# Optimization experiments

Measured on AMD Instinct MI355X. Metric: run time of the kernel, lower is better.

Reference implementation:

```python
import jax, jax.numpy as jnp
import numpy as np

B, T, D = 4, 2048, 1024
H, DK = 8, 64
EPS = 1e-6

def _xavier(key, shape):
    fan_in, fan_out = shape[1], shape[0]
    lim = float(np.sqrt(6.0 / (fan_in + fan_out)))
    return jax.random.uniform(key, shape, jnp.float32, -lim, lim)

def setup_inputs() -> dict:
    key = jax.random.key(0)
    ks = jax.random.split(key, 7)
    x = jax.random.normal(ks[0], (B, T, D), jnp.float32)
    W_Q = _xavier(ks[1], (H * DK, D))
    W_K = _xavier(ks[2], (H * DK, D))
    W_V = _xavier(ks[3], (H * DK, D))
    W_g_w = _xavier(ks[4], (H * DK, D))
    W_g_b = jax.random.normal(ks[5], (H * DK,), jnp.float32) * 0.02
    W_O = _xavier(ks[6], (D, H * DK))
    decay_log = jnp.zeros((H,), jnp.float32)
    return {"x": x, "W_Q": W_Q, "W_K": W_K, "W_V": W_V,
            "W_g_w": W_g_w, "W_g_b": W_g_b, "W_O": W_O,
            "decay_log": decay_log}

def _phi(u):
    # ELU + 1 feature map (positive)
    return jax.nn.elu(u) + 1.0

def reference(x, W_Q, W_K, W_V, W_g_w, W_g_b, W_O, decay_log):
    b, t, d = x.shape
    q = _phi((x @ W_Q.T).reshape(b, t, H, DK))
    k = _phi((x @ W_K.T).reshape(b, t, H, DK))
    v = (x @ W_V.T).reshape(b, t, H, DK)
    gamma = jax.nn.sigmoid(decay_log)           # [H]
    g4 = gamma[None, :, None, None]             # [1,H,1,1]
    g3 = gamma[None, :, None]                   # [1,H,1]

    # time-major for scan: [T,B,H,DK]
    qT = jnp.moveaxis(q, 1, 0)
    kT = jnp.moveaxis(k, 1, 0)
    vT = jnp.moveaxis(v, 1, 0)

    S0 = jnp.zeros((b, H, DK, DK), x.dtype)
    z0 = jnp.zeros((b, H, DK), x.dtype)

    def step(carry, inp):
        S, z = carry
        qt, kt, vt = inp
        S = g4 * S + jnp.einsum('bhi,bhj->bhij', kt, vt)
        z = g3 * z + kt
        num = jnp.einsum('bhij,bhi->bhj', S, qt)
        den = jnp.sum(z * qt, axis=-1, keepdims=True) + EPS
        return (S, z), num / den

    _, ys = jax.lax.scan(step, (S0, z0), (qT, kT, vT))  # ys: [T,B,H,DK]
    outputs = jnp.moveaxis(ys, 0, 1)                    # [B,T,H,DK]

    gate = jax.nn.sigmoid(x @ W_g_w.T + W_g_b).reshape(b, t, H, DK)
    y = (outputs * gate).reshape(b, t, H * DK)
    return y @ W_O.T
```

## Files before the change

### kernel.cpp

```cpp
#include <hip/hip_runtime.h>
#include <cstdint>
#include <cstddef>

#define B_   4
#define T_   2048
#define D_   1024
#define H_   8
#define DK_  64
#define HD_  512
#define CH_  64
#define NC_  32
#define EPS_ 1e-6f

typedef __attribute__((ext_vector_type(4))) float f32x4;
typedef __attribute__((ext_vector_type(8))) short s16x8;

__device__ __forceinline__ unsigned short f2bf(float f) {
    unsigned int x = __float_as_uint(f);
    unsigned int r = (x + 0x7FFFu + ((x >> 16) & 1u)) >> 16;
    return (unsigned short)r;
}
__device__ __forceinline__ float bf2f(unsigned short u) {
    return __uint_as_float(((unsigned int)u) << 16);
}
__device__ __forceinline__ void ld4(const float* p, float* o) {
    float4 v = *(const float4*)p; o[0]=v.x; o[1]=v.y; o[2]=v.z; o[3]=v.w;
}
__device__ __forceinline__ void gl_lds16(const unsigned short* g, unsigned short* l) {
    __builtin_amdgcn_global_load_lds(
        (const __attribute__((address_space(1))) unsigned int*)g,
        (__attribute__((address_space(3))) unsigned int*)l, 16, 0, 0);
}

__global__ __launch_bounds__(256) void k_cvt_all(
    const float* __restrict__ x,
    const float* __restrict__ wq, const float* __restrict__ wk,
    const float* __restrict__ wv, const float* __restrict__ wgw,
    const float* __restrict__ wo,
    unsigned short* __restrict__ xb,
    unsigned short* __restrict__ wqb, unsigned short* __restrict__ wkb,
    unsigned short* __restrict__ wvb, unsigned short* __restrict__ wgb,
    unsigned short* __restrict__ wob)
{
    int bid = blockIdx.x;
    const float* src; unsigned short* dst; int idx;
    if (bid < 8192) {
        src = x; dst = xb; idx = bid * 256 + threadIdx.x;
    } else {
        int r = bid - 8192;
        int w = r >> 9;
        idx = (r & 511) * 256 + threadIdx.x;
        switch (w) {
            case 0:  src = wq;  dst = wqb; break;
            case 1:  src = wk;  dst = wkb; break;
            case 2:  src = wv;  dst = wvb; break;
            case 3:  src = wgw; dst = wgb; break;
            default: src = wo;  dst = wob; break;
        }
    }
    float4 v = ((const float4*)src)[idx];
    ushort4 o;
    o.x = f2bf(v.x); o.y = f2bf(v.y); o.z = f2bf(v.z); o.w = f2bf(v.w);
    ((ushort4*)dst)[idx] = o;
}


__global__ __launch_bounds__(512, 2) void k_gemm_qkvg(
    const unsigned short* __restrict__ xb,
    const unsigned short* __restrict__ wqb, const unsigned short* __restrict__ wkb,
    const unsigned short* __restrict__ wvb, const unsigned short* __restrict__ wgb,
    const float* __restrict__ bias,
    unsigned short* __restrict__ qo, unsigned short* __restrict__ ko,
    unsigned short* __restrict__ vo, unsigned short* __restrict__ go)
{
    __shared__ unsigned short As[2][256 * 64];
    __shared__ unsigned short Bs[2][256 * 64];
    const int tid = threadIdx.x;
    const int id  = blockIdx.x;
    const int xcd = id & 7, per = id >> 3;
    const int mtile = xcd * 4 + (per & 3);
    const int ntile = per >> 2;
    const int which = ntile >> 1;
    const int nb    = ntile & 1;
    const int m0    = mtile * 256;
    const int n0    = nb * 256;
    const unsigned short* Wp = (which == 0) ? wqb : (which == 1) ? wkb : (which == 2) ? wvb : wgb;
    unsigned short* Op       = (which == 0) ? qo  : (which == 1) ? ko  : (which == 2) ? vo  : go;
    const int K = D_;
    const int NIT = K / 64;

    const int lane = tid & 63, wave = tid >> 6;
    const int wm = (wave >> 2) * 128, wn = (wave & 3) * 64;
    const int r16 = lane & 15, quad = lane >> 4;
    const int lrow = lane >> 3, lseg = lane & 7;
    const int sseg = lseg ^ lrow;
    const int rx   = r16 & 7;

    f32x4 acc[8][4];
    #pragma unroll
    for (int a = 0; a < 8; a++)
        #pragma unroll
        for (int b = 0; b < 4; b++) acc[a][b] = 0.0f;

    auto stageA = [&](int buf, int ko_) {
        #pragma unroll
        for (int i = 0; i < 4; i++) {
            int chunk = wave * 4 + i;
            int row = chunk * 8 + lrow;
            gl_lds16(xb + (size_t)(m0 + row) * K + ko_ + sseg * 8, &As[buf][chunk * 512]);
        }
    };
    auto stageB = [&](int buf, int ko_) {
        #pragma unroll
        for (int i = 0; i < 4; i++) {
            int chunk = wave * 4 + i;
            int row = chunk * 8 + lrow;
            gl_lds16(Wp + (size_t)(n0 + row) * K + ko_ + sseg * 8, &Bs[buf][chunk * 512]);
        }
    };
    auto rdA = [&](int buf, int row, int gb) -> s16x8 {
        return *(const s16x8*)&As[buf][row * 64 + (((gb + quad) ^ rx) << 3)];
    };
    auto rdB = [&](int buf, int row, int gb) -> s16x8 {
        return *(const s16x8*)&Bs[buf][row * 64 + (((gb + quad) ^ rx) << 3)];
    };

    stageA(0, 0); stageB(0, 0);
    for (int it = 0; it < NIT; ++it) {
        const int buf = it & 1;
        asm volatile("s_waitcnt vmcnt(0)" ::: "memory");
        __builtin_amdgcn_s_barrier();

        s16x8 af[4], bfr[4];
        #pragma unroll
        for (int mt = 0; mt < 4; mt++) af[mt]  = rdA(buf, wm + mt * 16 + r16, 0);
        #pragma unroll
        for (int nt = 0; nt < 4; nt++) bfr[nt] = rdB(buf, wn + nt * 16 + r16, 0);
        if (it + 1 < NIT) stageA(buf ^ 1, (it + 1) * 64);
        __builtin_amdgcn_s_barrier();
        asm volatile("s_waitcnt lgkmcnt(0)" ::: "memory");
        __builtin_amdgcn_sched_barrier(0);
        __builtin_amdgcn_s_setprio(1);
        #pragma unroll
        for (int mt = 0; mt < 4; mt++)
            #pragma unroll
            for (int nt = 0; nt < 4; nt++)
                acc[mt][nt] = __builtin_amdgcn_mfma_f32_16x16x32_bf16(af[mt], bfr[nt], acc[mt][nt], 0, 0, 0);
        __builtin_amdgcn_s_setprio(0);
        __builtin_amdgcn_s_barrier();

        #pragma unroll
        for (int mt = 0; mt < 4; mt++) af[mt] = rdA(buf, wm + (mt + 4) * 16 + r16, 0);
        if (it + 1 < NIT) stageB(buf ^ 1, (it + 1) * 64);
        __builtin_amdgcn_s_barrier();
        asm volatile("s_waitcnt lgkmcnt(0)" ::: "memory");
        __builtin_amdgcn_sched_barrier(0);
        __builtin_amdgcn_s_setprio(1);
        #pragma unroll
        for (int mt = 0; mt < 4; mt++)
            #pragma unroll
            for (int nt = 0; nt < 4; nt++)
                acc[mt + 4][nt] = __builtin_amdgcn_mfma_f32_16x16x32_bf16(af[mt], bfr[nt], acc[mt + 4][nt], 0, 0, 0);
        __builtin_amdgcn_s_setprio(0);
        __builtin_amdgcn_s_barrier();

        #pragma unroll
        for (int mt = 0; mt < 4; mt++) af[mt]  = rdA(buf, wm + mt * 16 + r16, 4);
        #pragma unroll
        for (int nt = 0; nt < 4; nt++) bfr[nt] = rdB(buf, wn + nt * 16 + r16, 4);
        __builtin_amdgcn_s_barrier();
        asm volatile("s_waitcnt lgkmcnt(0)" ::: "memory");
        __builtin_amdgcn_sched_barrier(0);
        __builtin_amdgcn_s_setprio(1);
        #pragma unroll
        for (int mt = 0; mt < 4; mt++)
            #pragma unroll
            for (int nt = 0; nt < 4; nt++)
                acc[mt][nt] = __builtin_amdgcn_mfma_f32_16x16x32_bf16(af[mt], bfr[nt], acc[mt][nt], 0, 0, 0);
        __builtin_amdgcn_s_setprio(0);
        __builtin_amdgcn_s_barrier();

        #pragma unroll
        for (int mt = 0; mt < 4; mt++) af[mt] = rdA(buf, wm + (mt + 4) * 16 + r16, 4);
        __builtin_amdgcn_s_barrier();
        asm volatile("s_waitcnt lgkmcnt(0)" ::: "memory");
        __builtin_amdgcn_sched_barrier(0);
        __builtin_amdgcn_s_setprio(1);
        #pragma unroll
        for (int mt = 0; mt < 4; mt++)
            #pragma unroll
            for (int nt = 0; nt < 4; nt++)
                acc[mt + 4][nt] = __builtin_amdgcn_mfma_f32_16x16x32_bf16(af[mt], bfr[nt], acc[mt + 4][nt], 0, 0, 0);
        __builtin_amdgcn_s_setprio(0);
        __builtin_amdgcn_s_barrier();
    }
    #pragma unroll
    for (int mt = 0; mt < 8; mt++) {
        #pragma unroll
        for (int nt = 0; nt < 4; nt++) {
            int col = n0 + wn + nt * 16 + r16;
            float bv = (which == 3) ? bias[col] : 0.0f;
            #pragma unroll
            for (int r = 0; r < 4; r++) {
                int row = m0 + wm + mt * 16 + quad * 4 + r;
                float v = acc[mt][nt][r];
                if (which <= 1)      v = (v > 0.0f) ? v + 1.0f : __builtin_expf(v);
                else if (which == 3) v = 1.0f / (1.0f + __builtin_expf(-(v + bv)));
                Op[(size_t)row * HD_ + col] = f2bf(v);
            }
        }
    }
}

__global__ __launch_bounds__(512, 2) void k_gemm_out(
    const unsigned short* __restrict__ ogb, const unsigned short* __restrict__ wob,
    float* __restrict__ y)
{
    __shared__ unsigned short As[2][256 * 64];
    __shared__ unsigned short Bs[2][128 * 64];
    const int tid = threadIdx.x;
    const int id  = blockIdx.x;
    const int xcd = id & 7, per = id >> 3;
    const int m0 = (xcd * 4 + (per & 3)) * 256;
    const int n0 = (per >> 2) * 128;
    const int K = HD_;
    const int NIT = K / 64;

    const int lane = tid & 63, wave = tid >> 6;
    const int wm = (wave >> 1) * 64, wn = (wave & 1) * 64;
    const int r16 = lane & 15, quad = lane >> 4;
    const int lrow = lane >> 3, lseg = lane & 7;
    const int sseg = lseg ^ lrow;
    const int rx   = r16 & 7;

    f32x4 acc[4][4];
    #pragma unroll
    for (int a = 0; a < 4; a++)
        #pragma unroll
        for (int b = 0; b < 4; b++) acc[a][b] = 0.0f;

    auto stageA = [&](int buf, int ko_) {
        #pragma unroll
        for (int i = 0; i < 4; i++) {
            int chunk = wave * 4 + i;
            int row = chunk * 8 + lrow;
            gl_lds16(ogb + (size_t)(m0 + row) * K + ko_ + sseg * 8, &As[buf][chunk * 512]);
        }
    };
    auto stageB = [&](int buf, int ko_) {
        #pragma unroll
        for (int i = 0; i < 2; i++) {
            int chunk = wave * 2 + i;
            int row = chunk * 8 + lrow;
            gl_lds16(wob + (size_t)(n0 + row) * K + ko_ + sseg * 8, &Bs[buf][chunk * 512]);
        }
    };
    auto rdA = [&](int buf, int row, int gb) -> s16x8 {
        return *(const s16x8*)&As[buf][row * 64 + (((gb + quad) ^ rx) << 3)];
    };
    auto rdB = [&](int buf, int row, int gb) -> s16x8 {
        return *(const s16x8*)&Bs[buf][row * 64 + (((gb + quad) ^ rx) << 3)];
    };

    stageA(0, 0); stageB(0, 0);
    for (int it = 0; it < NIT; ++it) {
        const int buf = it & 1;
        asm volatile("s_waitcnt vmcnt(0)" ::: "memory");
        __builtin_amdgcn_s_barrier();

        s16x8 af[4], bfr[4];
        #pragma unroll
        for (int mt = 0; mt < 4; mt++) af[mt]  = rdA(buf, wm + mt * 16 + r16, 0);
        #pragma unroll
        for (int nt = 0; nt < 4; nt++) bfr[nt] = rdB(buf, wn + nt * 16 + r16, 0);
        if (it + 1 < NIT) stageA(buf ^ 1, (it + 1) * 64);
        __builtin_amdgcn_s_barrier();
        asm volatile("s_waitcnt lgkmcnt(0)" ::: "memory");
        __builtin_amdgcn_sched_barrier(0);
        __builtin_amdgcn_s_setprio(1);
        #pragma unroll
        for (int mt = 0; mt < 4; mt++)
            #pragma unroll
            for (int nt = 0; nt < 4; nt++)
                acc[mt][nt] = __builtin_amdgcn_mfma_f32_16x16x32_bf16(af[mt], bfr[nt], acc[mt][nt], 0, 0, 0);
        __builtin_amdgcn_s_setprio(0);
        __builtin_amdgcn_s_barrier();

        #pragma unroll
        for (int mt = 0; mt < 4; mt++) af[mt]  = rdA(buf, wm + mt * 16 + r16, 4);
        #pragma unroll
        for (int nt = 0; nt < 4; nt++) bfr[nt] = rdB(buf, wn + nt * 16 + r16, 4);
        if (it + 1 < NIT) stageB(buf ^ 1, (it + 1) * 64);
        __builtin_amdgcn_s_barrier();
        asm volatile("s_waitcnt lgkmcnt(0)" ::: "memory");
        __builtin_amdgcn_sched_barrier(0);
        __builtin_amdgcn_s_setprio(1);
        #pragma unroll
        for (int mt = 0; mt < 4; mt++)
            #pragma unroll
            for (int nt = 0; nt < 4; nt++)
                acc[mt][nt] = __builtin_amdgcn_mfma_f32_16x16x32_bf16(af[mt], bfr[nt], acc[mt][nt], 0, 0, 0);
        __builtin_amdgcn_s_setprio(0);
        __builtin_amdgcn_s_barrier();
    }
    #pragma unroll
    for (int mt = 0; mt < 4; mt++)
        #pragma unroll
        for (int nt = 0; nt < 4; nt++) {
            int col = n0 + wn + nt * 16 + r16;
            #pragma unroll
            for (int r = 0; r < 4; r++) {
                int row = m0 + wm + mt * 16 + quad * 4 + r;
                y[(size_t)row * D_ + col] = acc[mt][nt][r];
            }
        }
}

__global__ __launch_bounds__(256) void k_chunk_sums(
    const unsigned short* __restrict__ Kb, const unsigned short* __restrict__ Vb,
    float* __restrict__ Ssum, float* __restrict__ zsum, const float* __restrict__ decay_log)
{
    __shared__ float kl[CH_ * 68];
    __shared__ float vl[CH_ * 68];
    const int tid = threadIdx.x;
    const int bc  = blockIdx.x;
    const int c   = bc & (NC_ - 1);
    const int bh  = bc >> 5;
    const int h   = bh & (H_ - 1);
    const int b   = bh >> 3;
    const float g  = 1.0f / (1.0f + __builtin_expf(-decay_log[h]));
    const float lg = __builtin_log2f(g);
    const int t0 = c * CH_;

    #pragma unroll
    for (int e = 0; e < 2; e++) {
        int lid = e * 256 + tid;
        int l = lid >> 3, d0 = (lid & 7) * 8;
        float w = __builtin_exp2f((float)(CH_ - 1 - l) * lg);
        size_t gidx = (size_t)(b * T_ + t0 + l) * HD_ + h * DK_ + d0;
        uint4 kraw = *(const uint4*)(Kb + gidx);
        uint4 vraw = *(const uint4*)(Vb + gidx);
        const unsigned short* kp = (const unsigned short*)&kraw;
        const unsigned short* vp = (const unsigned short*)&vraw;
        #pragma unroll
        for (int j = 0; j < 8; j++) {
            kl[l * 68 + d0 + j] = bf2f(kp[j]) * w;
            vl[l * 68 + d0 + j] = bf2f(vp[j]);
        }
    }
    __syncthreads();

    const int ti = tid >> 4, tj = tid & 15;
    const int i0 = ti * 4, j0 = tj * 4;
    float acc[4][4];
    #pragma unroll
    for (int r = 0; r < 4; r++)
        #pragma unroll
        for (int cc = 0; cc < 4; cc++) acc[r][cc] = 0.0f;

    for (int l = 0; l < CH_; l++) {
        float kv[4], vv[4];
        ld4(&kl[l * 68 + i0], kv);
        ld4(&vl[l * 68 + j0], vv);
        #pragma unroll
        for (int r = 0; r < 4; r++)
            #pragma unroll
            for (int cc = 0; cc < 4; cc++) acc[r][cc] += kv[r] * vv[cc];
    }
    size_t base = (size_t)bc * (DK_ * DK_);
    #pragma unroll
    for (int r = 0; r < 4; r++) {
        float4 st = make_float4(acc[r][0], acc[r][1], acc[r][2], acc[r][3]);
        *(float4*)&Ssum[base + (size_t)(i0 + r) * DK_ + j0] = st;
    }
    if (tid < DK_) {
        float s = 0.0f;
        for (int l = 0; l < CH_; l++) s += kl[l * 68 + tid];
        zsum[(size_t)bc * DK_ + tid] = s;
    }
}

__global__ __launch_bounds__(128) void k_chunk_scan(
    float* __restrict__ Ssum, float* __restrict__ zsum, const float* __restrict__ decay_log)
{
    const int tid = threadIdx.x;
    const int grp = blockIdx.x & 31;
    const int bh  = blockIdx.x >> 5;
    const int h   = bh & (H_ - 1);
    const float g  = 1.0f / (1.0f + __builtin_expf(-decay_log[h]));
    const float gC = __builtin_exp2f((float)CH_ * __builtin_log2f(g));
    int elem = grp * 128 + tid;
    float s = 0.0f;
    for (int c = 0; c < NC_; c++) {
        size_t idx = ((size_t)(bh * NC_ + c)) * 4096 + elem;
        float v = Ssum[idx];
        Ssum[idx] = s;
        s = gC * s + v;
    }
    if (grp == 0 && tid < DK_) {
        float z = 0.0f;
        for (int c = 0; c < NC_; c++) {
            size_t idx = ((size_t)(bh * NC_ + c)) * DK_ + tid;
            float v = zsum[idx];
            zsum[idx] = z;
            z = gC * z + v;
        }
    }
}

__global__ __launch_bounds__(256) void k_chunk_out(
    const unsigned short* __restrict__ Qb, const unsigned short* __restrict__ Kb,
    const unsigned short* __restrict__ Vb, const unsigned short* __restrict__ Gb,
    const float* __restrict__ Ssum, const float* __restrict__ zsum,
    unsigned short* __restrict__ OGb, const float* __restrict__ decay_log)
{
    __shared__ float BufA[CH_ * 68];
    __shared__ float BufB[CH_ * 68];
    __shared__ float BufC[CH_ * 68];
    __shared__ float den_l[CH_];
    __shared__ float zp_l[DK_];
    __shared__ float gpow[CH_ + 1];

    const int tid = threadIdx.x;
    const int bc  = blockIdx.x;
    const int c   = bc & (NC_ - 1);
    const int bh  = bc >> 5;
    const int h   = bh & (H_ - 1);
    const int b   = bh >> 3;
    const float g  = 1.0f / (1.0f + __builtin_expf(-decay_log[h]));
    const float lg = __builtin_log2f(g);
    const int t0 = c * CH_;

    if (tid <= CH_) gpow[tid] = __builtin_exp2f((float)tid * lg);
    if (tid < DK_)  zp_l[tid] = zsum[(size_t)bc * DK_ + tid];

    #pragma unroll
    for (int e = 0; e < 2; e++) {
        int lid = e * 256 + tid;
        int l = lid >> 3, d0 = (lid & 7) * 8;
        size_t gidx = (size_t)(b * T_ + t0 + l) * HD_ + h * DK_ + d0;
        uint4 qraw = *(const uint4*)(Qb + gidx);
        uint4 kraw = *(const uint4*)(Kb + gidx);
        const unsigned short* qp = (const unsigned short*)&qraw;
        const unsigned short* kp = (const unsigned short*)&kraw;
        #pragma unroll
        for (int j = 0; j < 8; j++) {
            BufA[(d0 + j) * 68 + l] = bf2f(qp[j]);
            BufB[(d0 + j) * 68 + l] = bf2f(kp[j]);
        }
    }
    {
        size_t base = (size_t)bc * 4096;
        #pragma unroll
        for (int e = 0; e < 4; e++) {
            int flat = (e * 256 + tid) * 4;
            int row = flat >> 6, c0 = flat & 63;
            *(float4*)&BufC[row * 68 + c0] = *(const float4*)&Ssum[base + flat];
        }
    }
    __syncthreads();

    const int ti = tid >> 4, tj = tid & 15;
    const int i0 = ti * 4, j0 = tj * 4;
    float sc[4][4], it[4][4];
    #pragma unroll
    for (int r = 0; r < 4; r++)
        #pragma unroll
        for (int cc = 0; cc < 4; cc++) { sc[r][cc] = 0.0f; it[r][cc] = 0.0f; }

    for (int d = 0; d < DK_; d++) {
        float qv[4], kv[4], sv[4];
        ld4(&BufA[d * 68 + i0], qv);
        ld4(&BufB[d * 68 + j0], kv);
        ld4(&BufC[d * 68 + j0], sv);
        #pragma unroll
        for (int r = 0; r < 4; r++)
            #pragma unroll
            for (int cc = 0; cc < 4; cc++) {
                sc[r][cc] += qv[r] * kv[cc];
                it[r][cc] += qv[r] * sv[cc];
            }
    }
    #pragma unroll
    for (int r = 0; r < 4; r++) {
        int i = i0 + r;
        #pragma unroll
        for (int cc = 0; cc < 4; cc++) {
            int jl = j0 + cc;
            sc[r][cc] = (jl <= i) ? sc[r][cc] * gpow[i - jl] : 0.0f;
            it[r][cc] *= gpow[i + 1];
        }
        float rs = sc[r][0] + sc[r][1] + sc[r][2] + sc[r][3];
        rs += __shfl_xor(rs, 1);
        rs += __shfl_xor(rs, 2);
        rs += __shfl_xor(rs, 4);
        rs += __shfl_xor(rs, 8);
        if (tj == 0) den_l[i] = rs;
    }
    __syncthreads();
    if (tid < DK_) {
        float dp = 0.0f;
        for (int d = 0; d < DK_; d++) dp += BufA[d * 68 + tid] * zp_l[d];
        den_l[tid] += gpow[tid + 1] * dp + EPS_;
    }
    __syncthreads();
    #pragma unroll
    for (int cc = 0; cc < 4; cc++) {
        float4 st = make_float4(sc[0][cc], sc[1][cc], sc[2][cc], sc[3][cc]);
        *(float4*)&BufA[(j0 + cc) * 68 + i0] = st;
    }
    #pragma unroll
    for (int e = 0; e < 2; e++) {
        int lid = e * 256 + tid;
        int l = lid >> 3, d0 = (lid & 7) * 8;
        size_t gidx = (size_t)(b * T_ + t0 + l) * HD_ + h * DK_ + d0;
        uint4 vraw = *(const uint4*)(Vb + gidx);
        const unsigned short* vp = (const unsigned short*)&vraw;
        #pragma unroll
        for (int j = 0; j < 8; j++) BufB[l * 68 + d0 + j] = bf2f(vp[j]);
    }
    __syncthreads();

    float og[4][4];
    #pragma unroll
    for (int r = 0; r < 4; r++)
        #pragma unroll
        for (int cc = 0; cc < 4; cc++) og[r][cc] = it[r][cc];

    for (int jl = 0; jl < CH_; jl++) {
        float scv[4], vv[4];
        ld4(&BufA[jl * 68 + i0], scv);
        ld4(&BufB[jl * 68 + j0], vv);
        #pragma unroll
        for (int r = 0; r < 4; r++)
            #pragma unroll
            for (int cc = 0; cc < 4; cc++) og[r][cc] += scv[r] * vv[cc];
    }
    #pragma unroll
    for (int r = 0; r < 4; r++) {
        int i = i0 + r;
        float rcp = 1.0f / den_l[i];
        size_t gidx = (size_t)(b * T_ + t0 + i) * HD_ + h * DK_ + j0;
        ushort4 graw = *(const ushort4*)(Gb + gidx);
        ushort4 o;
        o.x = f2bf(og[r][0] * rcp * bf2f(graw.x));
        o.y = f2bf(og[r][1] * rcp * bf2f(graw.y));
        o.z = f2bf(og[r][2] * rcp * bf2f(graw.z));
        o.w = f2bf(og[r][3] * rcp * bf2f(graw.w));
        *(ushort4*)(OGb + gidx) = o;
    }
}

extern "C" void kernel_launch(void* const* d_in, const int* in_sizes, int n_in,
                              void* d_out, int out_size, void* d_ws, size_t ws_size,
                              hipStream_t stream)
{
    (void)in_sizes; (void)n_in; (void)out_size; (void)ws_size;
    const float* x         = (const float*)d_in[0];
    const float* W_Q       = (const float*)d_in[1];
    const float* W_K       = (const float*)d_in[2];
    const float* W_V       = (const float*)d_in[3];
    const float* W_gw      = (const float*)d_in[4];
    const float* W_gb      = (const float*)d_in[5];
    const float* W_O       = (const float*)d_in[6];
    const float* decay_log = (const float*)d_in[7];
    float* y = (float*)d_out;

    char* ws = (char*)d_ws;
    size_t off = 0;
    auto alloc = [&](size_t bytes) { void* p = ws + off; off += (bytes + 255) & ~(size_t)255; return p; };
    unsigned short* xb   = (unsigned short*)alloc((size_t)B_ * T_ * D_ * 2);
    unsigned short* wqb  = (unsigned short*)alloc((size_t)HD_ * D_ * 2);
    unsigned short* wkb  = (unsigned short*)alloc((size_t)HD_ * D_ * 2);
    unsigned short* wvb  = (unsigned short*)alloc((size_t)HD_ * D_ * 2);
    unsigned short* wgb  = (unsigned short*)alloc((size_t)HD_ * D_ * 2);
    unsigned short* wob  = (unsigned short*)alloc((size_t)D_ * HD_ * 2);
    unsigned short* qb   = (unsigned short*)alloc((size_t)B_ * T_ * HD_ * 2);
    unsigned short* kb   = (unsigned short*)alloc((size_t)B_ * T_ * HD_ * 2);
    unsigned short* vb   = (unsigned short*)alloc((size_t)B_ * T_ * HD_ * 2);
    unsigned short* gb   = (unsigned short*)alloc((size_t)B_ * T_ * HD_ * 2);
    unsigned short* ogb  = (unsigned short*)alloc((size_t)B_ * T_ * HD_ * 2);
    float* Ssum = (float*)alloc((size_t)B_ * H_ * NC_ * DK_ * DK_ * 4);
    float* zsum = (float*)alloc((size_t)B_ * H_ * NC_ * DK_ * 4);

    k_cvt_all<<<8192 + 5 * 512, 256, 0, stream>>>(x, W_Q, W_K, W_V, W_gw, W_O,
                                                  xb, wqb, wkb, wvb, wgb, wob);
    k_gemm_qkvg<<<256, 512, 0, stream>>>(xb, wqb, wkb, wvb, wgb, W_gb, qb, kb, vb, gb);
    k_chunk_sums<<<B_ * H_ * NC_, 256, 0, stream>>>(kb, vb, Ssum, zsum, decay_log);
    k_chunk_scan<<<B_ * H_ * NC_, 128, 0, stream>>>(Ssum, zsum, decay_log);
    k_chunk_out<<<B_ * H_ * NC_, 256, 0, stream>>>(qb, kb, vb, gb, Ssum, zsum, ogb, decay_log);
    k_gemm_out<<<256, 512, 0, stream>>>(ogb, wob, y);
}
```

Before: 214.8 us.

## Split GEMM LDS tiles into K-halves and pipeline loads with partial vmcnt waits

Both bf16 GEMM kernels now store each 64-wide K slice as two 32-wide halves with a new XOR swizzle, and prefetch half-tiles up to two iterations ahead. The full vmcnt(0) drain is replaced by partial vmcnt waits, which lets global-to-LDS loads overlap the MFMA work across phases, and one barrier per iteration is dropped. The goal is to hide global memory latency in the projection GEMMs. The risk lies in the hand-counted vmcnt values and buffer reuse, where an ordering mistake could cause races.

```diff
diff --git a/kernel.cpp b/kernel.cpp
--- a/kernel.cpp
+++ b/kernel.cpp
@@ -73,8 +73,8 @@
     unsigned short* __restrict__ qo, unsigned short* __restrict__ ko,
     unsigned short* __restrict__ vo, unsigned short* __restrict__ go)
 {
-    __shared__ unsigned short As[2][256 * 64];
-    __shared__ unsigned short Bs[2][256 * 64];
+    __shared__ unsigned short As[2][2 * 256 * 32];
+    __shared__ unsigned short Bs[2][2 * 256 * 32];
     const int tid = threadIdx.x;
     const int id  = blockIdx.x;
     const int xcd = id & 7, per = id >> 3;
@@ -92,9 +92,7 @@
     const int lane = tid & 63, wave = tid >> 6;
     const int wm = (wave >> 2) * 128, wn = (wave & 3) * 64;
     const int r16 = lane & 15, quad = lane >> 4;
-    const int lrow = lane >> 3, lseg = lane & 7;
-    const int sseg = lseg ^ lrow;
-    const int rx   = r16 & 7;
+    const int srow = lane >> 2, sgran = lane & 3;
 
     f32x4 acc[8][4];
     #pragma unroll
@@ -102,41 +100,49 @@
         #pragma unroll
         for (int b = 0; b < 4; b++) acc[a][b] = 0.0f;
 
-    auto stageA = [&](int buf, int ko_) {
-        #pragma unroll
-        for (int i = 0; i < 4; i++) {
-            int chunk = wave * 4 + i;
-            int row = chunk * 8 + lrow;
-            gl_lds16(xb + (size_t)(m0 + row) * K + ko_ + sseg * 8, &As[buf][chunk * 512]);
-        }
-    };
-    auto stageB = [&](int buf, int ko_) {
-        #pragma unroll
-        for (int i = 0; i < 4; i++) {
-            int chunk = wave * 4 + i;
-            int row = chunk * 8 + lrow;
-            gl_lds16(Wp + (size_t)(n0 + row) * K + ko_ + sseg * 8, &Bs[buf][chunk * 512]);
-        }
-    };
-    auto rdA = [&](int buf, int row, int gb) -> s16x8 {
-        return *(const s16x8*)&As[buf][row * 64 + (((gb + quad) ^ rx) << 3)];
-    };
-    auto rdB = [&](int buf, int row, int gb) -> s16x8 {
-        return *(const s16x8*)&Bs[buf][row * 64 + (((gb + quad) ^ rx) << 3)];
-    };
-
-    stageA(0, 0); stageB(0, 0);
+    auto stageA = [&](int buf, int ko_, int kh) {
+        #pragma unroll
+        for (int j = 0; j < 2; j++) {
+            int chunk = wave * 2 + j;
+            int row = chunk * 16 + srow;
+            int g = sgran ^ ((row >> 1) & 3);
+            gl_lds16(xb + (size_t)(m0 + row) * K + ko_ + kh * 32 + g * 8,
+                     &As[buf][kh * 8192 + chunk * 512]);
+        }
+    };
+    auto stageB = [&](int buf, int ko_, int kh) {
+        #pragma unroll
+        for (int j = 0; j < 2; j++) {
+            int chunk = wave * 2 + j;
+            int row = chunk * 16 + srow;
+            int g = sgran ^ ((row >> 1) & 3);
+            gl_lds16(Wp + (size_t)(n0 + row) * K + ko_ + kh * 32 + g * 8,
+                     &Bs[buf][kh * 8192 + chunk * 512]);
+        }
+    };
+    auto rdA = [&](int buf, int kh, int row) -> s16x8 {
+        return *(const s16x8*)&As[buf][kh * 8192 + row * 32 + ((quad ^ ((row >> 1) & 3)) << 3)];
+    };
+    auto rdB = [&](int buf, int kh, int row) -> s16x8 {
+        return *(const s16x8*)&Bs[buf][kh * 8192 + row * 32 + ((quad ^ ((row >> 1) & 3)) << 3)];
+    };
+
+    stageA(0, 0, 0);  stageB(0, 0, 0);
+    stageA(0, 0, 1);  stageB(0, 0, 1);
+    stageA(1, 64, 0); stageB(1, 64, 0);
+
     for (int it = 0; it < NIT; ++it) {
         const int buf = it & 1;
-        asm volatile("s_waitcnt vmcnt(0)" ::: "memory");
+        if (it < NIT - 1) asm volatile("s_waitcnt vmcnt(8)" ::: "memory");
+        else              asm volatile("s_waitcnt vmcnt(4)" ::: "memory");
         __builtin_amdgcn_s_barrier();
 
         s16x8 af[4], bfr[4];
         #pragma unroll
-        for (int mt = 0; mt < 4; mt++) af[mt]  = rdA(buf, wm + mt * 16 + r16, 0);
-        #pragma unroll
-        for (int nt = 0; nt < 4; nt++) bfr[nt] = rdB(buf, wn + nt * 16 + r16, 0);
-        if (it + 1 < NIT) stageA(buf ^ 1, (it + 1) * 64);
+        for (int mt = 0; mt < 4; mt++) af[mt]  = rdA(buf, 0, wm + mt * 16 + r16);
+        #pragma unroll
+        for (int nt = 0; nt < 4; nt++) bfr[nt] = rdB(buf, 0, wn + nt * 16 + r16);
+        if (it + 1 < NIT) { stageA(buf ^ 1, (it + 1) * 64, 1); stageB(buf ^ 1, (it + 1) * 64, 1); }
         __builtin_amdgcn_s_barrier();
         asm volatile("s_waitcnt lgkmcnt(0)" ::: "memory");
         __builtin_amdgcn_sched_barrier(0);
@@ -150,8 +156,7 @@
         __builtin_amdgcn_s_barrier();
 
         #pragma unroll
-        for (int mt = 0; mt < 4; mt++) af[mt] = rdA(buf, wm + (mt + 4) * 16 + r16, 0);
-        if (it + 1 < NIT) stageB(buf ^ 1, (it + 1) * 64);
+        for (int mt = 0; mt < 4; mt++) af[mt] = rdA(buf, 0, wm + (mt + 4) * 16 + r16);
         __builtin_amdgcn_s_barrier();
         asm volatile("s_waitcnt lgkmcnt(0)" ::: "memory");
         __builtin_amdgcn_sched_barrier(0);
@@ -162,12 +167,15 @@
             for (int nt = 0; nt < 4; nt++)
                 acc[mt + 4][nt] = __builtin_amdgcn_mfma_f32_16x16x32_bf16(af[mt], bfr[nt], acc[mt + 4][nt], 0, 0, 0);
         __builtin_amdgcn_s_setprio(0);
-        __builtin_amdgcn_s_barrier();
-
-        #pragma unroll
-        for (int mt = 0; mt < 4; mt++) af[mt]  = rdA(buf, wm + mt * 16 + r16, 4);
-        #pragma unroll
-        for (int nt = 0; nt < 4; nt++) bfr[nt] = rdB(buf, wn + nt * 16 + r16, 4);
+        if (it < NIT - 1) asm volatile("s_waitcnt vmcnt(8)" ::: "memory");
+        else              asm volatile("s_waitcnt vmcnt(0)" ::: "memory");
+        __builtin_amdgcn_s_barrier();
+
+        #pragma unroll
+        for (int mt = 0; mt < 4; mt++) af[mt]  = rdA(buf, 1, wm + mt * 16 + r16);
+        #pragma unroll
+        for (int nt = 0; nt < 4; nt++) bfr[nt] = rdB(buf, 1, wn + nt * 16 + r16);
+        if (it + 2 < NIT) { stageA(buf, (it + 2) * 64, 0); stageB(buf, (it + 2) * 64, 0); }
         __builtin_amdgcn_s_barrier();
         asm volatile("s_waitcnt lgkmcnt(0)" ::: "memory");
         __builtin_amdgcn_sched_barrier(0);
@@ -181,7 +189,7 @@
         __builtin_amdgcn_s_barrier();
 
         #pragma unroll
-        for (int mt = 0; mt < 4; mt++) af[mt] = rdA(buf, wm + (mt + 4) * 16 + r16, 4);
+        for (int mt = 0; mt < 4; mt++) af[mt] = rdA(buf, 1, wm + (mt + 4) * 16 + r16);
         __builtin_amdgcn_s_barrier();
         asm volatile("s_waitcnt lgkmcnt(0)" ::: "memory");
         __builtin_amdgcn_sched_barrier(0);
@@ -192,7 +200,6 @@
             for (int nt = 0; nt < 4; nt++)
                 acc[mt + 4][nt] = __builtin_amdgcn_mfma_f32_16x16x32_bf16(af[mt], bfr[nt], acc[mt + 4][nt], 0, 0, 0);
         __builtin_amdgcn_s_setprio(0);
-        __builtin_amdgcn_s_barrier();
     }
     #pragma unroll
     for (int mt = 0; mt < 8; mt++) {
@@ -216,8 +223,8 @@
     const unsigned short* __restrict__ ogb, const unsigned short* __restrict__ wob,
     float* __restrict__ y)
 {
-    __shared__ unsigned short As[2][256 * 64];
-    __shared__ unsigned short Bs[2][128 * 64];
+    __shared__ unsigned short As[2][2 * 256 * 32];
+    __shared__ unsigned short Bs[2][2 * 128 * 32];
     const int tid = threadIdx.x;
     const int id  = blockIdx.x;
     const int xcd = id & 7, per = id >> 3;
@@ -229,9 +236,7 @@
     const int lane = tid & 63, wave = tid >> 6;
     const int wm = (wave >> 1) * 64, wn = (wave & 1) * 64;
     const int r16 = lane & 15, quad = lane >> 4;
-    const int lrow = lane >> 3, lseg = lane & 7;
-    const int sseg = lseg ^ lrow;
-    const int rx   = r16 & 7;
+    const int srow = lane >> 2, sgran = lane & 3;
 
     f32x4 acc[4][4];
     #pragma unroll
@@ -239,41 +244,46 @@
         #pragma unroll
         for (int b = 0; b < 4; b++) acc[a][b] = 0.0f;
 
-    auto stageA = [&](int buf, int ko_) {
-        #pragma unroll
-        for (int i = 0; i < 4; i++) {
-            int chunk = wave * 4 + i;
-            int row = chunk * 8 + lrow;
-            gl_lds16(ogb + (size_t)(m0 + row) * K + ko_ + sseg * 8, &As[buf][chunk * 512]);
-        }
-    };
-    auto stageB = [&](int buf, int ko_) {
-        #pragma unroll
-        for (int i = 0; i < 2; i++) {
-            int chunk = wave * 2 + i;
-            int row = chunk * 8 + lrow;
-            gl_lds16(wob + (size_t)(n0 + row) * K + ko_ + sseg * 8, &Bs[buf][chunk * 512]);
-        }
-    };
-    auto rdA = [&](int buf, int row, int gb) -> s16x8 {
-        return *(const s16x8*)&As[buf][row * 64 + (((gb + quad) ^ rx) << 3)];
-    };
-    auto rdB = [&](int buf, int row, int gb) -> s16x8 {
-        return *(const s16x8*)&Bs[buf][row * 64 + (((gb + quad) ^ rx) << 3)];
-    };
-
-    stageA(0, 0); stageB(0, 0);
+    auto stageA = [&](int buf, int ko_, int kh) {
+        #pragma unroll
+        for (int j = 0; j < 2; j++) {
+            int chunk = wave * 2 + j;
+            int row = chunk * 16 + srow;
+            int g = sgran ^ ((row >> 1) & 3);
+            gl_lds16(ogb + (size_t)(m0 + row) * K + ko_ + kh * 32 + g * 8,
+                     &As[buf][kh * 8192 + chunk * 512]);
+        }
+    };
+    auto stageB = [&](int buf, int ko_, int kh) {
+        int chunk = wave;
+        int row = chunk * 16 + srow;
+        int g = sgran ^ ((row >> 1) & 3);
+        gl_lds16(wob + (size_t)(n0 + row) * K + ko_ + kh * 32 + g * 8,
+                 &Bs[buf][kh * 4096 + chunk * 512]);
+    };
+    auto rdA = [&](int buf, int kh, int row) -> s16x8 {
+        return *(const s16x8*)&As[buf][kh * 8192 + row * 32 + ((quad ^ ((row >> 1) & 3)) << 3)];
+    };
+    auto rdB = [&](int buf, int kh, int row) -> s16x8 {
+        return *(const s16x8*)&Bs[buf][kh * 4096 + row * 32 + ((quad ^ ((row >> 1) & 3)) << 3)];
+    };
+
+    stageA(0, 0, 0);  stageB(0, 0, 0);
+    stageA(0, 0, 1);  stageB(0, 0, 1);
+    stageA(1, 64, 0); stageB(1, 64, 0);
+
     for (int it = 0; it < NIT; ++it) {
         const int buf = it & 1;
-        asm volatile("s_waitcnt vmcnt(0)" ::: "memory");
+        if (it < NIT - 1) asm volatile("s_waitcnt vmcnt(6)" ::: "memory");
+        else              asm volatile("s_waitcnt vmcnt(3)" ::: "memory");
         __builtin_amdgcn_s_barrier();
 
         s16x8 af[4], bfr[4];
         #pragma unroll
-        for (int mt = 0; mt < 4; mt++) af[mt]  = rdA(buf, wm + mt * 16 + r16, 0);
-        #pragma unroll
-        for (int nt = 0; nt < 4; nt++) bfr[nt] = rdB(buf, wn + nt * 16 + r16, 0);
-        if (it + 1 < NIT) stageA(buf ^ 1, (it + 1) * 64);
+        for (int mt = 0; mt < 4; mt++) af[mt]  = rdA(buf, 0, wm + mt * 16 + r16);
+        #pragma unroll
+        for (int nt = 0; nt < 4; nt++) bfr[nt] = rdB(buf, 0, wn + nt * 16 + r16);
+        if (it + 1 < NIT) { stageA(buf ^ 1, (it + 1) * 64, 1); stageB(buf ^ 1, (it + 1) * 64, 1); }
         __builtin_amdgcn_s_barrier();
         asm volatile("s_waitcnt lgkmcnt(0)" ::: "memory");
         __builtin_amdgcn_sched_barrier(0);
@@ -284,13 +294,15 @@
             for (int nt = 0; nt < 4; nt++)
                 acc[mt][nt] = __builtin_amdgcn_mfma_f32_16x16x32_bf16(af[mt], bfr[nt], acc[mt][nt], 0, 0, 0);
         __builtin_amdgcn_s_setprio(0);
-        __builtin_amdgcn_s_barrier();
-
-        #pragma unroll
-        for (int mt = 0; mt < 4; mt++) af[mt]  = rdA(buf, wm + mt * 16 + r16, 4);
-        #pragma unroll
-        for (int nt = 0; nt < 4; nt++) bfr[nt] = rdB(buf, wn + nt * 16 + r16, 4);
-        if (it + 1 < NIT) stageB(buf ^ 1, (it + 1) * 64);
+        if (it < NIT - 1) asm volatile("s_waitcnt vmcnt(6)" ::: "memory");
+        else              asm volatile("s_waitcnt vmcnt(0)" ::: "memory");
+        __builtin_amdgcn_s_barrier();
+
+        #pragma unroll
+        for (int mt = 0; mt < 4; mt++) af[mt]  = rdA(buf, 1, wm + mt * 16 + r16);
+        #pragma unroll
+        for (int nt = 0; nt < 4; nt++) bfr[nt] = rdB(buf, 1, wn + nt * 16 + r16);
+        if (it + 2 < NIT) { stageA(buf, (it + 2) * 64, 0); stageB(buf, (it + 2) * 64, 0); }
         __builtin_amdgcn_s_barrier();
         asm volatile("s_waitcnt lgkmcnt(0)" ::: "memory");
         __builtin_amdgcn_sched_barrier(0);
@@ -301,7 +313,6 @@
             for (int nt = 0; nt < 4; nt++)
                 acc[mt][nt] = __builtin_amdgcn_mfma_f32_16x16x32_bf16(af[mt], bfr[nt], acc[mt][nt], 0, 0, 0);
         __builtin_amdgcn_s_setprio(0);
-        __builtin_amdgcn_s_barrier();
     }
     #pragma unroll
     for (int mt = 0; mt < 4; mt++)
```

Result: no change. 217.7 us (+1.4%).

## Fuse chunk sums, scan and output into one sequential MFMA kernel per head

Applied to the files above, without the earlier changes.

Replaces the three chunked linear-attention kernels with a single kernel per (batch, head) that walks all chunks sequentially. It keeps the running state and normaliser in shared memory and uses bf16 MFMA for the intra-chunk scores, state contribution and state update. This removes the global Ssum/zsum round trips and two launches. In exchange, the grid drops to 32 blocks, each serialized over 32 chunks, and the state is rounded to bf16 for the MFMA inputs.

```diff
diff --git a/kernel.cpp b/kernel.cpp
--- a/kernel.cpp
+++ b/kernel.cpp
@@ -22,9 +22,6 @@
 }
 __device__ __forceinline__ float bf2f(unsigned short u) {
     return __uint_as_float(((unsigned int)u) << 16);
-}
-__device__ __forceinline__ void ld4(const float* p, float* o) {
-    float4 v = *(const float4*)p; o[0]=v.x; o[1]=v.y; o[2]=v.z; o[3]=v.w;
 }
 __device__ __forceinline__ void gl_lds16(const unsigned short* g, unsigned short* l) {
     __builtin_amdgcn_global_load_lds(
@@ -64,7 +61,6 @@
     ((ushort4*)dst)[idx] = o;
 }
 
-
 __global__ __launch_bounds__(512, 2) void k_gemm_qkvg(
     const unsigned short* __restrict__ xb,
     const unsigned short* __restrict__ wqb, const unsigned short* __restrict__ wkb,
@@ -316,238 +312,197 @@
         }
 }
 
-__global__ __launch_bounds__(256) void k_chunk_sums(
-    const unsigned short* __restrict__ Kb, const unsigned short* __restrict__ Vb,
-    float* __restrict__ Ssum, float* __restrict__ zsum, const float* __restrict__ decay_log)
+__global__ __launch_bounds__(512) void k_chunk_fused(
+    const unsigned short* __restrict__ Qb, const unsigned short* __restrict__ Kb,
+    const unsigned short* __restrict__ Vb, const unsigned short* __restrict__ Gb,
+    unsigned short* __restrict__ OGb, const float* __restrict__ decay_log)
 {
-    __shared__ float kl[CH_ * 68];
-    __shared__ float vl[CH_ * 68];
+    __shared__ unsigned short ql[64 * 72];
+    __shared__ unsigned short kl[64 * 72];
+    __shared__ unsigned short kt[64 * 72];
+    __shared__ unsigned short vt[64 * 72];
+    __shared__ unsigned short pl[64 * 72];
+    __shared__ float stf[64 * 68];
+    __shared__ float den2[2][64];
+    __shared__ float den_l[64];
+    __shared__ float zl[64];
+    __shared__ float gpow[CH_ + 1];
+
     const int tid = threadIdx.x;
-    const int bc  = blockIdx.x;
-    const int c   = bc & (NC_ - 1);
-    const int bh  = bc >> 5;
+    const int bh  = blockIdx.x;
     const int h   = bh & (H_ - 1);
     const int b   = bh >> 3;
     const float g  = 1.0f / (1.0f + __builtin_expf(-decay_log[h]));
     const float lg = __builtin_log2f(g);
-    const int t0 = c * CH_;
-
-    #pragma unroll
-    for (int e = 0; e < 2; e++) {
-        int lid = e * 256 + tid;
-        int l = lid >> 3, d0 = (lid & 7) * 8;
-        float w = __builtin_exp2f((float)(CH_ - 1 - l) * lg);
-        size_t gidx = (size_t)(b * T_ + t0 + l) * HD_ + h * DK_ + d0;
-        uint4 kraw = *(const uint4*)(Kb + gidx);
-        uint4 vraw = *(const uint4*)(Vb + gidx);
-        const unsigned short* kp = (const unsigned short*)&kraw;
-        const unsigned short* vp = (const unsigned short*)&vraw;
-        #pragma unroll
-        for (int j = 0; j < 8; j++) {
-            kl[l * 68 + d0 + j] = bf2f(kp[j]) * w;
-            vl[l * 68 + d0 + j] = bf2f(vp[j]);
-        }
-    }
+    const float gC = __builtin_exp2f((float)CH_ * lg);
+
+    if (tid <= CH_) gpow[tid] = __builtin_exp2f((float)tid * lg);
+    if (tid < DK_)  zl[tid] = 0.0f;
+    for (int i = tid; i < 64 * 68; i += 512) stf[i] = 0.0f;
+
+    const int lane = tid & 63, wave = tid >> 6;
+    const int r16 = lane & 15, quad = lane >> 4;
+    const int ib = wave & 3, half = wave >> 2;
+
+    const int lt_ = tid >> 3, ld0 = (tid & 7) * 8;
+    const float wdec = __builtin_exp2f((float)(CH_ - 1 - lt_) * lg);
+
     __syncthreads();
 
-    const int ti = tid >> 4, tj = tid & 15;
-    const int i0 = ti * 4, j0 = tj * 4;
-    float acc[4][4];
-    #pragma unroll
-    for (int r = 0; r < 4; r++)
-        #pragma unroll
-        for (int cc = 0; cc < 4; cc++) acc[r][cc] = 0.0f;
-
-    for (int l = 0; l < CH_; l++) {
-        float kv[4], vv[4];
-        ld4(&kl[l * 68 + i0], kv);
-        ld4(&vl[l * 68 + j0], vv);
-        #pragma unroll
-        for (int r = 0; r < 4; r++)
-            #pragma unroll
-            for (int cc = 0; cc < 4; cc++) acc[r][cc] += kv[r] * vv[cc];
-    }
-    size_t base = (size_t)bc * (DK_ * DK_);
-    #pragma unroll
-    for (int r = 0; r < 4; r++) {
-        float4 st = make_float4(acc[r][0], acc[r][1], acc[r][2], acc[r][3]);
-        *(float4*)&Ssum[base + (size_t)(i0 + r) * DK_ + j0] = st;
-    }
-    if (tid < DK_) {
-        float s = 0.0f;
-        for (int l = 0; l < CH_; l++) s += kl[l * 68 + tid];
-        zsum[(size_t)bc * DK_ + tid] = s;
-    }
-}
-
-__global__ __launch_bounds__(128) void k_chunk_scan(
-    float* __restrict__ Ssum, float* __restrict__ zsum, const float* __restrict__ decay_log)
-{
-    const int tid = threadIdx.x;
-    const int grp = blockIdx.x & 31;
-    const int bh  = blockIdx.x >> 5;
-    const int h   = bh & (H_ - 1);
-    const float g  = 1.0f / (1.0f + __builtin_expf(-decay_log[h]));
-    const float gC = __builtin_exp2f((float)CH_ * __builtin_log2f(g));
-    int elem = grp * 128 + tid;
-    float s = 0.0f;
-    for (int c = 0; c < NC_; c++) {
-        size_t idx = ((size_t)(bh * NC_ + c)) * 4096 + elem;
-        float v = Ssum[idx];
-        Ssum[idx] = s;
-        s = gC * s + v;
-    }
-    if (grp == 0 && tid < DK_) {
-        float z = 0.0f;
-        for (int c = 0; c < NC_; c++) {
-            size_t idx = ((size_t)(bh * NC_ + c)) * DK_ + tid;
-            float v = zsum[idx];
-            zsum[idx] = z;
-            z = gC * z + v;
-        }
-    }
-}
-
-__global__ __launch_bounds__(256) void k_chunk_out(
-    const unsigned short* __restrict__ Qb, const unsigned short* __restrict__ Kb,
-    const unsigned short* __restrict__ Vb, const unsigned short* __restrict__ Gb,
-    const float* __restrict__ Ssum, const float* __restrict__ zsum,
-    unsigned short* __restrict__ OGb, const float* __restrict__ decay_log)
-{
-    __shared__ float BufA[CH_ * 68];
-    __shared__ float BufB[CH_ * 68];
-    __shared__ float BufC[CH_ * 68];
-    __shared__ float den_l[CH_];
-    __shared__ float zp_l[DK_];
-    __shared__ float gpow[CH_ + 1];
-
-    const int tid = threadIdx.x;
-    const int bc  = blockIdx.x;
-    const int c   = bc & (NC_ - 1);
-    const int bh  = bc >> 5;
-    const int h   = bh & (H_ - 1);
-    const int b   = bh >> 3;
-    const float g  = 1.0f / (1.0f + __builtin_expf(-decay_log[h]));
-    const float lg = __builtin_log2f(g);
-    const int t0 = c * CH_;
-
-    if (tid <= CH_) gpow[tid] = __builtin_exp2f((float)tid * lg);
-    if (tid < DK_)  zp_l[tid] = zsum[(size_t)bc * DK_ + tid];
-
-    #pragma unroll
-    for (int e = 0; e < 2; e++) {
-        int lid = e * 256 + tid;
-        int l = lid >> 3, d0 = (lid & 7) * 8;
-        size_t gidx = (size_t)(b * T_ + t0 + l) * HD_ + h * DK_ + d0;
-        uint4 qraw = *(const uint4*)(Qb + gidx);
-        uint4 kraw = *(const uint4*)(Kb + gidx);
-        const unsigned short* qp = (const unsigned short*)&qraw;
-        const unsigned short* kp = (const unsigned short*)&kraw;
-        #pragma unroll
-        for (int j = 0; j < 8; j++) {
-            BufA[(d0 + j) * 68 + l] = bf2f(qp[j]);
-            BufB[(d0 + j) * 68 + l] = bf2f(kp[j]);
-        }
-    }
-    {
-        size_t base = (size_t)bc * 4096;
-        #pragma unroll
-        for (int e = 0; e < 4; e++) {
-            int flat = (e * 256 + tid) * 4;
-            int row = flat >> 6, c0 = flat & 63;
-            *(float4*)&BufC[row * 68 + c0] = *(const float4*)&Ssum[base + flat];
-        }
-    }
-    __syncthreads();
-
-    const int ti = tid >> 4, tj = tid & 15;
-    const int i0 = ti * 4, j0 = tj * 4;
-    float sc[4][4], it[4][4];
-    #pragma unroll
-    for (int r = 0; r < 4; r++)
-        #pragma unroll
-        for (int cc = 0; cc < 4; cc++) { sc[r][cc] = 0.0f; it[r][cc] = 0.0f; }
-
-    for (int d = 0; d < DK_; d++) {
-        float qv[4], kv[4], sv[4];
-        ld4(&BufA[d * 68 + i0], qv);
-        ld4(&BufB[d * 68 + j0], kv);
-        ld4(&BufC[d * 68 + j0], sv);
-        #pragma unroll
-        for (int r = 0; r < 4; r++)
-            #pragma unroll
-            for (int cc = 0; cc < 4; cc++) {
-                sc[r][cc] += qv[r] * kv[cc];
-                it[r][cc] += qv[r] * sv[cc];
-            }
-    }
-    #pragma unroll
-    for (int r = 0; r < 4; r++) {
-        int i = i0 + r;
-        #pragma unroll
-        for (int cc = 0; cc < 4; cc++) {
-            int jl = j0 + cc;
-            sc[r][cc] = (jl <= i) ? sc[r][cc] * gpow[i - jl] : 0.0f;
-            it[r][cc] *= gpow[i + 1];
-        }
-        float rs = sc[r][0] + sc[r][1] + sc[r][2] + sc[r][3];
-        rs += __shfl_xor(rs, 1);
-        rs += __shfl_xor(rs, 2);
-        rs += __shfl_xor(rs, 4);
-        rs += __shfl_xor(rs, 8);
-        if (tj == 0) den_l[i] = rs;
-    }
-    __syncthreads();
-    if (tid < DK_) {
-        float dp = 0.0f;
-        for (int d = 0; d < DK_; d++) dp += BufA[d * 68 + tid] * zp_l[d];
-        den_l[tid] += gpow[tid + 1] * dp + EPS_;
-    }
-    __syncthreads();
-    #pragma unroll
-    for (int cc = 0; cc < 4; cc++) {
-        float4 st = make_float4(sc[0][cc], sc[1][cc], sc[2][cc], sc[3][cc]);
-        *(float4*)&BufA[(j0 + cc) * 68 + i0] = st;
-    }
-    #pragma unroll
-    for (int e = 0; e < 2; e++) {
-        int lid = e * 256 + tid;
-        int l = lid >> 3, d0 = (lid & 7) * 8;
-        size_t gidx = (size_t)(b * T_ + t0 + l) * HD_ + h * DK_ + d0;
-        uint4 vraw = *(const uint4*)(Vb + gidx);
-        const unsigned short* vp = (const unsigned short*)&vraw;
-        #pragma unroll
-        for (int j = 0; j < 8; j++) BufB[l * 68 + d0 + j] = bf2f(vp[j]);
-    }
-    __syncthreads();
-
-    float og[4][4];
-    #pragma unroll
-    for (int r = 0; r < 4; r++)
-        #pragma unroll
-        for (int cc = 0; cc < 4; cc++) og[r][cc] = it[r][cc];
-
-    for (int jl = 0; jl < CH_; jl++) {
-        float scv[4], vv[4];
-        ld4(&BufA[jl * 68 + i0], scv);
-        ld4(&BufB[jl * 68 + j0], vv);
-        #pragma unroll
-        for (int r = 0; r < 4; r++)
-            #pragma unroll
-            for (int cc = 0; cc < 4; cc++) og[r][cc] += scv[r] * vv[cc];
-    }
-    #pragma unroll
-    for (int r = 0; r < 4; r++) {
-        int i = i0 + r;
-        float rcp = 1.0f / den_l[i];
-        size_t gidx = (size_t)(b * T_ + t0 + i) * HD_ + h * DK_ + j0;
-        ushort4 graw = *(const ushort4*)(Gb + gidx);
-        ushort4 o;
-        o.x = f2bf(og[r][0] * rcp * bf2f(graw.x));
-        o.y = f2bf(og[r][1] * rcp * bf2f(graw.y));
-        o.z = f2bf(og[r][2] * rcp * bf2f(graw.z));
-        o.w = f2bf(og[r][3] * rcp * bf2f(graw.w));
-        *(ushort4*)(OGb + gidx) = o;
+    size_t g0 = (size_t)(b * T_ + lt_) * HD_ + h * DK_ + ld0;
+    uint4 qr = *(const uint4*)(Qb + g0);
+    uint4 kr = *(const uint4*)(Kb + g0);
+    uint4 vr = *(const uint4*)(Vb + g0);
+
+    for (int c = 0; c < NC_; ++c) {
+        const int t0 = c * CH_;
+        *(uint4*)&ql[lt_ * 72 + ld0] = qr;
+        *(uint4*)&kl[lt_ * 72 + ld0] = kr;
+        {
+            const unsigned short* kp = (const unsigned short*)&kr;
+            const unsigned short* vp = (const unsigned short*)&vr;
+            #pragma unroll
+            for (int j = 0; j < 8; j++) {
+                kt[(ld0 + j) * 72 + lt_] = f2bf(bf2f(kp[j]) * wdec);
+                vt[(ld0 + j) * 72 + lt_] = vp[j];
+            }
+        }
+        __syncthreads();
+        if (c + 1 < NC_) {
+            size_t gn = (size_t)(b * T_ + (c + 1) * CH_ + lt_) * HD_ + h * DK_ + ld0;
+            qr = *(const uint4*)(Qb + gn);
+            kr = *(const uint4*)(Kb + gn);
+            vr = *(const uint4*)(Vb + gn);
+        }
+
+        f32x4 sc2[2];
+        sc2[0] = 0.0f; sc2[1] = 0.0f;
+        #pragma unroll
+        for (int t2 = 0; t2 < 2; t2++) {
+            int lt = 2 * half + t2;
+            #pragma unroll
+            for (int ks = 0; ks < 2; ks++) {
+                s16x8 af  = *(const s16x8*)&ql[(16 * ib + r16) * 72 + ks * 32 + quad * 8];
+                s16x8 bf_ = *(const s16x8*)&kl[(16 * lt + r16) * 72 + ks * 32 + quad * 8];
+                sc2[t2] = __builtin_amdgcn_mfma_f32_16x16x32_bf16(af, bf_, sc2[t2], 0, 0, 0);
+            }
+        }
+        float rs[4] = {0.0f, 0.0f, 0.0f, 0.0f};
+        #pragma unroll
+        for (int t2 = 0; t2 < 2; t2++) {
+            int l = 16 * (2 * half + t2) + r16;
+            #pragma unroll
+            for (int rr = 0; rr < 4; rr++) {
+                int i = 16 * ib + quad * 4 + rr;
+                int diff = i - l;
+                float val = (diff >= 0) ? sc2[t2][rr] * gpow[diff] : 0.0f;
+                unsigned short pb = f2bf(val);
+                pl[i * 72 + l] = pb;
+                rs[rr] += bf2f(pb);
+            }
+        }
+        #pragma unroll
+        for (int rr = 0; rr < 4; rr++) {
+            float v_ = rs[rr];
+            v_ += __shfl_xor(v_, 1);
+            v_ += __shfl_xor(v_, 2);
+            v_ += __shfl_xor(v_, 4);
+            v_ += __shfl_xor(v_, 8);
+            if (r16 == 0) den2[half][16 * ib + quad * 4 + rr] = v_;
+        }
+        __syncthreads();
+
+        f32x4 og2[2];
+        #pragma unroll
+        for (int t2 = 0; t2 < 2; t2++) {
+            int jt = 2 * half + t2;
+            f32x4 o = 0.0f;
+            #pragma unroll
+            for (int ks = 0; ks < 2; ks++) {
+                s16x8 af = *(const s16x8*)&ql[(16 * ib + r16) * 72 + ks * 32 + quad * 8];
+                const float* sp = &stf[(16 * jt + r16) * 68 + ks * 32 + quad * 8];
+                s16x8 bf_;
+                #pragma unroll
+                for (int e = 0; e < 8; e++) bf_[e] = (short)f2bf(sp[e]);
+                o = __builtin_amdgcn_mfma_f32_16x16x32_bf16(af, bf_, o, 0, 0, 0);
+            }
+            og2[t2] = o;
+        }
+        #pragma unroll
+        for (int t2 = 0; t2 < 2; t2++)
+            #pragma unroll
+            for (int rr = 0; rr < 4; rr++)
+                og2[t2][rr] *= gpow[16 * ib + quad * 4 + rr + 1];
+        #pragma unroll
+        for (int t2 = 0; t2 < 2; t2++) {
+            int jt = 2 * half + t2;
+            #pragma unroll
+            for (int ks = 0; ks < 2; ks++) {
+                s16x8 af  = *(const s16x8*)&pl[(16 * ib + r16) * 72 + ks * 32 + quad * 8];
+                s16x8 bf_ = *(const s16x8*)&vt[(16 * jt + r16) * 72 + ks * 32 + quad * 8];
+                og2[t2] = __builtin_amdgcn_mfma_f32_16x16x32_bf16(af, bf_, og2[t2], 0, 0, 0);
+            }
+        }
+        f32x4 ds2[2];
+        #pragma unroll
+        for (int t2 = 0; t2 < 2; t2++) {
+            int it_ = 2 * half + t2;
+            f32x4 dd = 0.0f;
+            #pragma unroll
+            for (int ks = 0; ks < 2; ks++) {
+                s16x8 af  = *(const s16x8*)&vt[(16 * ib + r16) * 72 + ks * 32 + quad * 8];
+                s16x8 bf_ = *(const s16x8*)&kt[(16 * it_ + r16) * 72 + ks * 32 + quad * 8];
+                dd = __builtin_amdgcn_mfma_f32_16x16x32_bf16(af, bf_, dd, 0, 0, 0);
+            }
+            ds2[t2] = dd;
+        }
+        if (tid < DK_) {
+            float dp = 0.0f;
+            #pragma unroll
+            for (int d8 = 0; d8 < 8; d8++) {
+                uint4 qq = *(const uint4*)&ql[tid * 72 + d8 * 8];
+                const unsigned short* qp = (const unsigned short*)&qq;
+                #pragma unroll
+                for (int e = 0; e < 8; e++) dp += bf2f(qp[e]) * zl[d8 * 8 + e];
+            }
+            den_l[tid] = den2[0][tid] + den2[1][tid] + gpow[tid + 1] * dp + EPS_;
+        }
+        __syncthreads();
+
+        #pragma unroll
+        for (int t2 = 0; t2 < 2; t2++) {
+            int it_ = 2 * half + t2;
+            #pragma unroll
+            for (int rr = 0; rr < 4; rr++) {
+                int j = 16 * ib + quad * 4 + rr;
+                float* sp = &stf[j * 68 + 16 * it_ + r16];
+                *sp = gC * (*sp) + ds2[t2][rr];
+            }
+        }
+        if (tid < DK_) {
+            float zs = 0.0f;
+            #pragma unroll
+            for (int l8 = 0; l8 < 8; l8++) {
+                uint4 kk = *(const uint4*)&kt[tid * 72 + l8 * 8];
+                const unsigned short* kp = (const unsigned short*)&kk;
+                #pragma unroll
+                for (int e = 0; e < 8; e++) zs += bf2f(kp[e]);
+            }
+            zl[tid] = gC * zl[tid] + zs;
+        }
+        #pragma unroll
+        for (int t2 = 0; t2 < 2; t2++) {
+            int j = 16 * (2 * half + t2) + r16;
+            #pragma unroll
+            for (int rr = 0; rr < 4; rr++) {
+                int i = 16 * ib + quad * 4 + rr;
+                float rcp = 1.0f / den_l[i];
+                size_t ga = (size_t)(b * T_ + t0 + i) * HD_ + h * DK_ + j;
+                float gate = bf2f(Gb[ga]);
+                OGb[ga] = f2bf(og2[t2][rr] * rcp * gate);
+            }
+        }
+        __syncthreads();
     }
 }
 
@@ -580,14 +535,10 @@
     unsigned short* vb   = (unsigned short*)alloc((size_t)B_ * T_ * HD_ * 2);
     unsigned short* gb   = (unsigned short*)alloc((size_t)B_ * T_ * HD_ * 2);
     unsigned short* ogb  = (unsigned short*)alloc((size_t)B_ * T_ * HD_ * 2);
-    float* Ssum = (float*)alloc((size_t)B_ * H_ * NC_ * DK_ * DK_ * 4);
-    float* zsum = (float*)alloc((size_t)B_ * H_ * NC_ * DK_ * 4);
 
     k_cvt_all<<<8192 + 5 * 512, 256, 0, stream>>>(x, W_Q, W_K, W_V, W_gw, W_O,
                                                   xb, wqb, wkb, wvb, wgb, wob);
     k_gemm_qkvg<<<256, 512, 0, stream>>>(xb, wqb, wkb, wvb, wgb, W_gb, qb, kb, vb, gb);
-    k_chunk_sums<<<B_ * H_ * NC_, 256, 0, stream>>>(kb, vb, Ssum, zsum, decay_log);
-    k_chunk_scan<<<B_ * H_ * NC_, 128, 0, stream>>>(Ssum, zsum, decay_log);
-    k_chunk_out<<<B_ * H_ * NC_, 256, 0, stream>>>(qb, kb, vb, gb, Ssum, zsum, ogb, decay_log);
+    k_chunk_fused<<<B_ * H_, 512, 0, stream>>>(qb, kb, vb, gb, ogb, decay_log);
     k_gemm_out<<<256, 512, 0, stream>>>(ogb, wob, y);
 }
```

Measured after the change: 311.1 us. 1.45x slower.
